# Kernel tuning notes

Hardware: AMD Instinct MI355X
Metric: run time of the kernel (lower is better)

## Reference

```python
import jax, jax.numpy as jnp
import numpy as np

B, N, HID, H, DH, NB = 4, 4096, 768, 12, 64, 266
EPS = 1e-4


def softmax_kernel(data, proj, is_query):
    # data: [B,H,N,DH], proj: [NB,DH]. FAVOR+ positive softmax features.
    d = data.shape[-1]
    ratio = proj.shape[0] ** -0.5
    dn = d ** -0.25  # data normalizer
    data_dash = jnp.einsum('bhnd,jd->bhnj', data * dn, proj)  # [B,H,N,NB]
    diag = 0.5 * jnp.sum((data * dn) ** 2, axis=-1, keepdims=True)  # [B,H,N,1]
    if is_query:
        m = jnp.max(data_dash, axis=-1, keepdims=True)
    else:
        m = jnp.max(data_dash, axis=(-1, -2), keepdims=True)
    return ratio * (jnp.exp(data_dash - diag - m) + EPS)


def setup_inputs() -> dict:
    key = jax.random.key(0)
    ks = jax.random.split(key, 8)
    s = HID ** -0.5
    return {
        'hidden_states': jax.random.normal(ks[0], (B, N, HID), jnp.float32),
        'Wq': jax.random.normal(ks[1], (HID, HID), jnp.float32) * s,
        'bq': jnp.zeros((HID,), jnp.float32),
        'Wk': jax.random.normal(ks[2], (HID, HID), jnp.float32) * s,
        'bk': jnp.zeros((HID,), jnp.float32),
        'Wv': jax.random.normal(ks[3], (HID, HID), jnp.float32) * s,
        'bv': jnp.zeros((HID,), jnp.float32),
        'proj': jax.random.normal(ks[4], (NB, DH), jnp.float32),
    }


def reference(hidden_states, Wq, bq, Wk, bk, Wv, bv, proj):
    def heads(x):  # [B,N,HID] -> [B,H,N,DH]
        return x.reshape(B, N, H, DH).transpose(0, 2, 1, 3)

    q = heads(hidden_states @ Wq.T + bq)
    k = heads(hidden_states @ Wk.T + bk)
    v = heads(hidden_states @ Wv.T + bv)

    qp = softmax_kernel(q, proj, True)   # [B,H,N,NB]
    kp = softmax_kernel(k, proj, False)  # [B,H,N,NB]

    # non-causal linear attention: out = q' (k'^T v) / (q' sum_n k')
    k_sum = jnp.sum(kp, axis=2)                               # [B,H,NB]
    d_inv = 1.0 / jnp.einsum('bhnj,bhj->bhn', qp, k_sum)      # [B,H,N]
    ctx = jnp.einsum('bhnj,bhnd->bhjd', kp, v)                # [B,H,NB,DH]
    out = jnp.einsum('bhnj,bhjd->bhnd', qp, ctx) * d_inv[..., None]

    return out.transpose(0, 2, 1, 3).reshape(B, N, HID)
```

## Files before the change

kernel.cpp:

```cpp
#include <hip/hip_runtime.h>
#include <hip/hip_bf16.h>
#include <stdint.h>

#define B_   4
#define N_   4096
#define HID_ 768
#define H_   12
#define DH_  64
#define NB_  266
#define NBP_ 288
#define EPS_ 1e-4f
#define RATIO_ 0.06131393f
#define CSL_  ((size_t)48 * DH_ * NBP_)
#define KSL_  ((size_t)48 * NBP_)

typedef unsigned short u16;
typedef __attribute__((ext_vector_type(8))) short short8;
typedef __attribute__((ext_vector_type(4))) float floatx4;

__device__ __forceinline__ u16 f2b(float f) {
  __hip_bfloat16 h = __float2bfloat16(f);
  return *reinterpret_cast<u16*>(&h);
}
__device__ __forceinline__ float b2f(u16 u) {
  union { unsigned u; float f; } x; x.u = ((unsigned)u) << 16; return x.f;
}
__device__ __forceinline__ unsigned fmap(float x) {
  unsigned u = __float_as_uint(x);
  return (u & 0x80000000u) ? ~u : (u | 0x80000000u);
}
__device__ __forceinline__ float funmap(unsigned u) {
  unsigned b = (u & 0x80000000u) ? (u & 0x7FFFFFFFu) : ~u;
  return __uint_as_float(b);
}
__device__ __forceinline__ void gl16(const u16* g, u16* l) {
  __builtin_amdgcn_global_load_lds(
      (const __attribute__((address_space(1))) void*)g,
      (__attribute__((address_space(3))) void*)l, 16, 0, 0);
}

__global__ __launch_bounds__(256) void k_prep(
    const float4* __restrict__ hs, const float4* __restrict__ Wq,
    const float4* __restrict__ Wk, const float4* __restrict__ Wv,
    const float* __restrict__ proj,
    uint2* __restrict__ hsb, uint2* __restrict__ wb3, u16* __restrict__ projb,
    float* __restrict__ Vdz, unsigned* __restrict__ mbuf) {
  int blk = blockIdx.x;
  const int t = threadIdx.x;
  if (blk < 12288) {
    int i = blk * 256 + t;
    float4 v = hs[i];
    union { u16 s[4]; uint2 u; } pk;
    pk.s[0] = f2b(v.x); pk.s[1] = f2b(v.y); pk.s[2] = f2b(v.z); pk.s[3] = f2b(v.w);
    hsb[i] = pk.u;
    return;
  }
  blk -= 12288;
  if (blk < 1728) {
    int i = blk * 256 + t;
    int sel = i / 147456, j = i - sel * 147456;
    const float4* s = (sel == 0) ? Wq : (sel == 1) ? Wk : Wv;
    float4 v = s[j];
    union { u16 s4[4]; uint2 u; } pk;
    pk.s4[0] = f2b(v.x); pk.s4[1] = f2b(v.y); pk.s4[2] = f2b(v.z); pk.s4[3] = f2b(v.w);
    wb3[i] = pk.u;
    return;
  }
  blk -= 1728;
  if (blk < 72) {
    int i = blk * 256 + t;
    int j = i / DH_, d = i - j * DH_;
    float v = (j < NB_) ? proj[j * DH_ + d] * 0.35355339059327373f : 0.f;
    projb[i] = f2b(v);
    return;
  }
  blk -= 72;
  if (blk < 12) {
    int i = blk * 256 + t;
    Vdz[i] = 0.f;
    return;
  }
  if (t < B_ * H_) mbuf[t] = 0u;
}

__global__ __launch_bounds__(256) void k_qkv3(
    const u16* __restrict__ hsb, const u16* __restrict__ wb,
    const float* __restrict__ bq, const float* __restrict__ bk, const float* __restrict__ bv,
    u16* __restrict__ qb, u16* __restrict__ kb, u16* __restrict__ vT,
    float* __restrict__ diagk, float* __restrict__ Vd) {
  __shared__ u16 lds[3 * 8192];
  const int m0 = blockIdx.x * 128;
  const int bn = blockIdx.y;
  const int sel = bn / 6;
  const int or0 = (bn % 6) * 128;
  const u16* W = wb + (size_t)sel * HID_ * HID_;
  const int t = threadIdx.x, lane = t & 63, wv = t >> 6;
  const int lm = lane & 15, lq = lane >> 4;
  const int wr = (wv >> 1) * 64, wc = (wv & 1) * 64;
  const int srow = t >> 2;
  const int scol = ((t & 3) ^ ((t >> 3) & 3)) * 8;
  const u16* gA0 = hsb + (size_t)(m0 + srow) * HID_ + scol;
  const u16* gB0 = W + (size_t)(or0 + srow) * HID_ + scol;
  u16* lb = lds + wv * 512;
  const int slotc = (lq ^ ((lm >> 1) & 3)) * 8;
  const int aoff = (wr + lm) * 32 + slotc;
  const int boff = 4096 + (wc + lm) * 32 + slotc;

  floatx4 acc[4][4];
#pragma unroll
  for (int mt = 0; mt < 4; mt++)
#pragma unroll
    for (int nt = 0; nt < 4; nt++) acc[mt][nt] = (floatx4){0.f, 0.f, 0.f, 0.f};

#define STAGE_QKV(kt)                                            \
  {                                                              \
    const int k0_ = (kt) * 32;                                   \
    u16* l_ = lb + ((kt) % 3) * 8192;                            \
    gl16(gA0 + k0_, l_);                                         \
    gl16(gA0 + 64 * HID_ + k0_, l_ + 2048);                      \
    gl16(gB0 + k0_, l_ + 4096);                                  \
    gl16(gB0 + 64 * HID_ + k0_, l_ + 6144);                      \
  }

  STAGE_QKV(0);
  STAGE_QKV(1);
  asm volatile("s_waitcnt vmcnt(4)" ::: "memory");
  __builtin_amdgcn_s_barrier();

  for (int kt = 0; kt < 24; ++kt) {
    if (kt + 2 < 24) STAGE_QKV(kt + 2);
    const u16* bufA = lds + (kt % 3) * 8192;
    short8 af[4], bf[4];
#pragma unroll
    for (int mt = 0; mt < 4; mt++) af[mt] = *(const short8*)&bufA[aoff + mt * 512];
#pragma unroll
    for (int nt = 0; nt < 4; nt++) bf[nt] = *(const short8*)&bufA[boff + nt * 512];
    __builtin_amdgcn_s_setprio(1);
#pragma unroll
    for (int mt = 0; mt < 4; mt++)
#pragma unroll
      for (int nt = 0; nt < 4; nt++)
        acc[mt][nt] = __builtin_amdgcn_mfma_f32_16x16x32_bf16(af[mt], bf[nt], acc[mt][nt], 0, 0, 0);
    __builtin_amdgcn_s_setprio(0);
    if (kt < 22) asm volatile("s_waitcnt vmcnt(4)" ::: "memory");
    else         asm volatile("s_waitcnt vmcnt(0)" ::: "memory");
    __builtin_amdgcn_s_barrier();
  }
#undef STAGE_QKV

  if (sel == 0) {
#pragma unroll
    for (int nt = 0; nt < 4; nt++) {
      int lc = or0 + wc + nt * 16 + lm;
      float bb = bq[lc];
#pragma unroll
      for (int mt = 0; mt < 4; mt++) {
        int rowb = m0 + wr + mt * 16 + lq * 4;
#pragma unroll
        for (int r = 0; r < 4; r++)
          qb[(size_t)(rowb + r) * HID_ + lc] = f2b(acc[mt][nt][r] + bb);
      }
    }
  } else if (sel == 1) {
    float dsq[4][4];
#pragma unroll
    for (int mt = 0; mt < 4; mt++)
#pragma unroll
      for (int r = 0; r < 4; r++) dsq[mt][r] = 0.f;
#pragma unroll
    for (int nt = 0; nt < 4; nt++) {
      int lc = or0 + wc + nt * 16 + lm;
      float bb = bk[lc];
#pragma unroll
      for (int mt = 0; mt < 4; mt++) {
        int rowb = m0 + wr + mt * 16 + lq * 4;
#pragma unroll
        for (int r = 0; r < 4; r++) {
          u16 hv = f2b(acc[mt][nt][r] + bb);
          kb[(size_t)(rowb + r) * HID_ + lc] = hv;
          float fv = b2f(hv);
          dsq[mt][r] += fv * fv;
        }
      }
    }
    const int bh0 = (m0 >> 12) * H_ + ((or0 + wc) >> 6);
#pragma unroll
    for (int mt = 0; mt < 4; mt++)
#pragma unroll
      for (int r = 0; r < 4; r++) {
        float v = dsq[mt][r];
        v += __shfl_xor(v, 1); v += __shfl_xor(v, 2);
        v += __shfl_xor(v, 4); v += __shfl_xor(v, 8);
        if (lm == 0) {
          int rowb = m0 + wr + mt * 16 + lq * 4 + r;
          diagk[(size_t)bh0 * N_ + (rowb & 4095)] = 0.0625f * v;
        }
      }
  } else {
    const int hh = (or0 + wc) >> 6;
#pragma unroll
    for (int nt = 0; nt < 4; nt++) {
      int lc = or0 + wc + nt * 16 + lm;
      int dv = nt * 16 + lm;
      float bb = bv[lc];
      float vs = 0.f;
#pragma unroll
      for (int mt = 0; mt < 4; mt++) {
        int rowbase = m0 + wr + mt * 16 + lq * 4;
        int b = rowbase >> 12, n = rowbase & 4095;
        union { u16 s[4]; uint2 u; } pk;
#pragma unroll
        for (int r = 0; r < 4; r++) {
          float fv = acc[mt][nt][r] + bb;
          vs += fv;
          pk.s[r] = f2b(fv);
        }
        *(uint2*)(vT + ((size_t)(b * H_ + hh) * DH_ + dv) * N_ + n) = pk.u;
      }
      vs += __shfl_xor(vs, 16);
      vs += __shfl_xor(vs, 32);
      if (lq == 0) atomicAdd(&Vd[((m0 >> 12) * H_ + hh) * DH_ + dv], vs);
    }
  }
}

__global__ __launch_bounds__(256) void k_ctx6(
    const u16* __restrict__ kb, const u16* __restrict__ vT, const u16* __restrict__ projb,
    const float* __restrict__ diagk,
    float* __restrict__ ksumS8, float* __restrict__ ctxTf8, unsigned* __restrict__ mbuf) {
  __shared__ u16 kpl[32 * 72];
  __shared__ float kred[4][2][16];
  const int orig = blockIdx.x;
  const int lg = (orig & 7) * 432 + (orig >> 3);
  const int bhjb = lg >> 3, ns = lg & 7;
  const int bh = bhjb / 9, jb = bhjb - bh * 9;
  const int j0 = jb * 32;
  const int nbeg = ns * 512;
  const int b = bh / H_, h = bh - b * H_;
  const int t = threadIdx.x, lane = t & 63, wv = t >> 6;
  const int lm = lane & 15, lq = lane >> 4;
  const bool vj0 = (j0 + lm) < NB_;
  const bool vj1 = (j0 + 16 + lm) < NB_;
  short8 bp00, bp01, bp10, bp11;
  {
    const u16* pp = projb + (j0 + lm) * DH_ + lq * 8;
    bp00 = *(const short8*)pp;
    bp01 = *(const short8*)(pp + 32);
    pp += 16 * DH_;
    bp10 = *(const short8*)pp;
    bp11 = *(const short8*)(pp + 32);
  }
  const u16* kbB = kb + (size_t)(b * N_) * HID_ + h * DH_;
  const u16* vTb = vT + ((size_t)bh * DH_ + wv * 16 + lm) * N_;
  const float* dgB = diagk + (size_t)bh * N_;
  floatx4 acc0 = (floatx4){0.f,0.f,0.f,0.f}, acc1 = (floatx4){0.f,0.f,0.f,0.f};
  float kacc0 = 0.f, kacc1 = 0.f;
  float am = -3e38f;
  const u16* kr0 = kbB + (size_t)(nbeg + wv * 16 + lm) * HID_ + lq * 8;
  short8 af0 = *(const short8*)kr0;
  short8 af1 = *(const short8*)(kr0 + 32);
  floatx4 dg4 = *(const floatx4*)(dgB + nbeg + wv * 16 + lq * 4);

  for (int n64 = nbeg; n64 < nbeg + 512; n64 += 64) {
    __syncthreads();
    const int nn = (n64 + 64 < nbeg + 512) ? n64 + 64 : nbeg;
    const u16* krn = kbB + (size_t)(nn + wv * 16 + lm) * HID_ + lq * 8;
    short8 nf0 = *(const short8*)krn;
    short8 nf1 = *(const short8*)(krn + 32);
    floatx4 nd = *(const floatx4*)(dgB + nn + wv * 16 + lq * 4);
    short8 av0 = *(const short8*)(vTb + n64 + lq * 8);
    short8 av1 = *(const short8*)(vTb + n64 + 32 + lq * 8);
    {
      floatx4 a = __builtin_amdgcn_mfma_f32_16x16x32_bf16(af0, bp00, (floatx4){0.f,0.f,0.f,0.f}, 0, 0, 0);
      a = __builtin_amdgcn_mfma_f32_16x16x32_bf16(af1, bp01, a, 0, 0, 0);
      union { u16 s[4]; uint2 u; } pk;
      float kss = 0.f;
#pragma unroll
      for (int r = 0; r < 4; r++) {
        float tv = __expf(a[r] - dg4[r]);
        if (vj0) am = fmaxf(am, a[r]);
        kss += tv;
        pk.s[r] = f2b(tv);
      }
      kacc0 += kss;
      *(uint2*)&kpl[lm * 72 + wv * 16 + lq * 4] = pk.u;
      a = __builtin_amdgcn_mfma_f32_16x16x32_bf16(af0, bp10, (floatx4){0.f,0.f,0.f,0.f}, 0, 0, 0);
      a = __builtin_amdgcn_mfma_f32_16x16x32_bf16(af1, bp11, a, 0, 0, 0);
      kss = 0.f;
#pragma unroll
      for (int r = 0; r < 4; r++) {
        float tv = __expf(a[r] - dg4[r]);
        if (vj1) am = fmaxf(am, a[r]);
        kss += tv;
        pk.s[r] = f2b(tv);
      }
      kacc1 += kss;
      *(uint2*)&kpl[(16 + lm) * 72 + wv * 16 + lq * 4] = pk.u;
    }
    __syncthreads();
    {
      short8 bf = *(const short8*)&kpl[lm * 72 + lq * 8];
      acc0 = __builtin_amdgcn_mfma_f32_16x16x32_bf16(av0, bf, acc0, 0, 0, 0);
      bf = *(const short8*)&kpl[(16 + lm) * 72 + lq * 8];
      acc1 = __builtin_amdgcn_mfma_f32_16x16x32_bf16(av0, bf, acc1, 0, 0, 0);
      bf = *(const short8*)&kpl[lm * 72 + 32 + lq * 8];
      acc0 = __builtin_amdgcn_mfma_f32_16x16x32_bf16(av1, bf, acc0, 0, 0, 0);
      bf = *(const short8*)&kpl[(16 + lm) * 72 + 32 + lq * 8];
      acc1 = __builtin_amdgcn_mfma_f32_16x16x32_bf16(av1, bf, acc1, 0, 0, 0);
    }
    af0 = nf0; af1 = nf1; dg4 = nd;
  }
  {
    float v0 = kacc0; v0 += __shfl_xor(v0, 16); v0 += __shfl_xor(v0, 32);
    float v1 = kacc1; v1 += __shfl_xor(v1, 16); v1 += __shfl_xor(v1, 32);
    if (lq == 0) { kred[wv][0][lm] = v0; kred[wv][1][lm] = v1; }
  }
  __syncthreads();
  if (t < 32) {
    int jh = t >> 4, l = t & 15;
    ksumS8[(size_t)ns * KSL_ + bh * NBP_ + j0 + t] =
        kred[0][jh][l] + kred[1][jh][l] + kred[2][jh][l] + kred[3][jh][l];
  }
  {
    float* cb = ctxTf8 + (size_t)ns * CSL_ + ((size_t)bh * DH_ + wv * 16 + lq * 4) * NBP_ + j0 + lm;
#pragma unroll
    for (int r = 0; r < 4; r++) {
      cb[(size_t)r * NBP_] = acc0[r];
      cb[(size_t)r * NBP_ + 16] = acc1[r];
    }
  }
#pragma unroll
  for (int o = 1; o < 64; o <<= 1) am = fmaxf(am, __shfl_xor(am, o));
  if (lane == 0) atomicMax(&mbuf[bh], fmap(am));
}

__global__ __launch_bounds__(256) void k_fink(
    const float* __restrict__ ksumS8, const unsigned* __restrict__ mbuf,
    float* __restrict__ ksumf, float* __restrict__ Ck) {
  __shared__ float cks[4];
  const int bh = blockIdx.x;
  const int t = threadIdx.x;
  const float em = __expf(-funmap(mbuf[bh]));
  float ck = 0.f;
  for (int j = t; j < NBP_; j += 256) {
    const float* p = ksumS8 + bh * NBP_ + j;
    float s = p[0];
#pragma unroll
    for (int ns = 1; ns < 8; ns++) s += p[(size_t)ns * KSL_];
    float kv = (j < NB_) ? RATIO_ * (em * s + EPS_ * 4096.0f) : 0.f;
    ksumf[bh * NBP_ + j] = kv;
    ck += kv;
  }
#pragma unroll
  for (int o = 1; o < 64; o <<= 1) ck += __shfl_xor(ck, o);
  if ((t & 63) == 0) cks[t >> 6] = ck;
  __syncthreads();
  if (t == 0) Ck[bh] = ((cks[0] + cks[1]) + cks[2]) + cks[3];
}

__global__ __launch_bounds__(256) void k_finc(
    const float* __restrict__ ctxTf8, const float* __restrict__ Vd,
    const unsigned* __restrict__ mbuf,
    u16* __restrict__ ctxb, float* __restrict__ Cc) {
  __shared__ float red[4];
  const int d = blockIdx.x, bh = blockIdx.y;
  const int t = threadIdx.x;
  const float em = __expf(-funmap(mbuf[bh]));
  const float vd = Vd[bh * DH_ + d];
  const size_t rb = ((size_t)bh * DH_ + d) * NBP_;
  float csum = 0.f;
  for (int j = t; j < NBP_; j += 256) {
    const float* p = ctxTf8 + rb + j;
    float s = p[0];
#pragma unroll
    for (int ns = 1; ns < 8; ns++) s += p[(size_t)ns * CSL_];
    float c = (j < NB_) ? RATIO_ * (em * s + EPS_ * vd) : 0.f;
    csum += c;
    ctxb[rb + j] = f2b(c);
  }
#pragma unroll
  for (int o = 1; o < 64; o <<= 1) csum += __shfl_xor(csum, o);
  if ((t & 63) == 0) red[t >> 6] = csum;
  __syncthreads();
  if (t == 0) Cc[bh * DH_ + d] = ((red[0] + red[1]) + red[2]) + red[3];
}

__global__ __launch_bounds__(256) void k_out5(
    const u16* __restrict__ qb, const u16* __restrict__ projb,
    const u16* __restrict__ ctxb, const float* __restrict__ ksumf,
    const float* __restrict__ Cc, const float* __restrict__ Ck,
    float* __restrict__ outp) {
  __shared__ u16 qpl[4][16][296];
  const int bh = blockIdx.y, b = bh / H_, h = bh - b * H_;
  const int t = threadIdx.x, lane = t & 63, wv = t >> 6;
  const int lm = lane & 15, lq = lane >> 4;
  const int row0 = blockIdx.x * 64 + wv * 16;
  const u16* cb = ctxb + (size_t)bh * DH_ * NBP_;
  const float* ksb = ksumf + bh * NBP_;
  float ksv[17];
#pragma unroll
  for (int ct = 0; ct < 17; ct++) ksv[ct] = ksb[ct * 16 + lm];
  const float ckv = Ck[bh];

  const u16* prow = qb + (size_t)(b * N_ + row0 + lm) * HID_ + h * DH_ + lq * 8;
  short8 af0 = *(const short8*)prow;
  short8 af1 = *(const short8*)(prow + 32);
  float rs = 0.f;
#pragma unroll
  for (int i = 0; i < 8; i++) { float f = b2f(((const u16*)&af0)[i]); rs += f * f; }
#pragma unroll
  for (int i = 0; i < 8; i++) { float f = b2f(((const u16*)&af1)[i]); rs += f * f; }
  rs += __shfl_xor(rs, 16);
  rs += __shfl_xor(rs, 32);
  float dg[4];
#pragma unroll
  for (int r = 0; r < 4; r++) dg[r] = 0.0625f * __shfl(rs, lq * 4 + r);

  float tmax[4] = {0.f, 0.f, 0.f, 0.f};
  float skp[4] = {0.f, 0.f, 0.f, 0.f};
#pragma unroll
  for (int ct = 0; ct < 17; ct++) {
    const u16* pp = projb + (ct * 16 + lm) * DH_ + lq * 8;
    short8 bf0 = *(const short8*)pp;
    short8 bf1 = *(const short8*)(pp + 32);
    floatx4 a = __builtin_amdgcn_mfma_f32_16x16x32_bf16(af0, bf0, (floatx4){0.f,0.f,0.f,0.f}, 0, 0, 0);
    a = __builtin_amdgcn_mfma_f32_16x16x32_bf16(af1, bf1, a, 0, 0, 0);
    bool valid = (ct < 16) || (lm < 10);
#pragma unroll
    for (int r = 0; r < 4; r++) {
      float tv = __expf(a[r] - dg[r]);
      if (valid) tmax[r] = fmaxf(tmax[r], tv);
      skp[r] += tv * ksv[ct];
      qpl[wv][lq * 4 + r][ct * 16 + lm] = f2b(tv);
    }
  }
#pragma unroll
  for (int r = 0; r < 4; r++) qpl[wv][lq * 4 + r][272 + lm] = 0;
#pragma unroll
  for (int o = 1; o < 16; o <<= 1) {
#pragma unroll
    for (int r = 0; r < 4; r++) {
      tmax[r] = fmaxf(tmax[r], __shfl_xor(tmax[r], o));
      skp[r] += __shfl_xor(skp[r], o);
    }
  }
  float alpha[4], beta[4];
#pragma unroll
  for (int r = 0; r < 4; r++) {
    float s = __expf(-dg[r]) / tmax[r];
    float dinv = 1.f / (s * skp[r] + EPS_ * ckv);
    alpha[r] = s * dinv;
    beta[r] = EPS_ * dinv;
  }

  floatx4 ao[4];
#pragma unroll
  for (int dt = 0; dt < 4; dt++) ao[dt] = (floatx4){0.f, 0.f, 0.f, 0.f};
#pragma unroll
  for (int ks9 = 0; ks9 < 9; ks9++) {
    short8 aq = *(const short8*)&qpl[wv][lm][ks9 * 32 + lq * 8];
#pragma unroll
    for (int dt = 0; dt < 4; dt++) {
      short8 bc = *(const short8*)(cb + (size_t)(dt * 16 + lm) * NBP_ + ks9 * 32 + lq * 8);
      ao[dt] = __builtin_amdgcn_mfma_f32_16x16x32_bf16(aq, bc, ao[dt], 0, 0, 0);
    }
  }
#pragma unroll
  for (int dt = 0; dt < 4; dt++) {
    float ccd = Cc[bh * DH_ + dt * 16 + lm];
#pragma unroll
    for (int r = 0; r < 4; r++) {
      int n = row0 + lq * 4 + r;
      outp[((size_t)(b * N_ + n)) * HID_ + h * DH_ + dt * 16 + lm] =
          ao[dt][r] * alpha[r] + ccd * beta[r];
    }
  }
}

extern "C" void kernel_launch(void* const* d_in, const int* in_sizes, int n_in,
                              void* d_out, int out_size, void* d_ws, size_t ws_size,
                              hipStream_t stream) {
  (void)in_sizes; (void)n_in; (void)out_size; (void)ws_size;
  const float* hs   = (const float*)d_in[0];
  const float* Wq   = (const float*)d_in[1];
  const float* bq   = (const float*)d_in[2];
  const float* Wk   = (const float*)d_in[3];
  const float* bk   = (const float*)d_in[4];
  const float* Wv   = (const float*)d_in[5];
  const float* bv   = (const float*)d_in[6];
  const float* proj = (const float*)d_in[7];

  char* w = (char*)d_ws;
  u16* hsb   = (u16*)w;  w += (size_t)16384 * 768 * 2;
  u16* wb3   = (u16*)w;  w += (size_t)3 * 768 * 768 * 2;
  u16* projb = (u16*)w;  w += (size_t)NBP_ * 64 * 2;
  u16* qb    = (u16*)w;  w += (size_t)16384 * 768 * 2;
  u16* kb    = (u16*)w;  w += (size_t)16384 * 768 * 2;
  u16* vT    = (u16*)w;  w += (size_t)48 * DH_ * N_ * 2;
  float* ksumS8 = (float*)w; w += (size_t)8 * KSL_ * 4;
  float* ksumf  = (float*)w; w += (size_t)48 * NBP_ * 4;
  float* diagk  = (float*)w; w += (size_t)48 * N_ * 4;
  float* ctxTf8 = (float*)w; w += (size_t)8 * CSL_ * 4;
  u16* ctxTb = (u16*)w;  w += (size_t)48 * DH_ * NBP_ * 2;
  float* Vd   = (float*)w; w += (size_t)48 * DH_ * 4;
  float* Cc   = (float*)w; w += (size_t)48 * DH_ * 4;
  float* Ck   = (float*)w; w += (size_t)48 * 4;
  unsigned* mbuf = (unsigned*)w;

  hipLaunchKernelGGL(k_prep, dim3(14101), dim3(256), 0, stream,
                     (const float4*)hs, (const float4*)Wq, (const float4*)Wk, (const float4*)Wv,
                     proj, (uint2*)hsb, (uint2*)wb3, projb, Vd, mbuf);
  hipLaunchKernelGGL(k_qkv3, dim3(128, 18), dim3(256), 0, stream, hsb, wb3, bq, bk, bv, qb, kb, vT, diagk, Vd);
  hipLaunchKernelGGL(k_ctx6, dim3(3456), dim3(256), 0, stream, kb, vT, projb, diagk, ksumS8, ctxTf8, mbuf);
  hipLaunchKernelGGL(k_fink, dim3(48), dim3(256), 0, stream, ksumS8, mbuf, ksumf, Ck);
  hipLaunchKernelGGL(k_finc, dim3(64, 48), dim3(256), 0, stream, ctxTf8, Vd, mbuf, ctxTb, Cc);
  hipLaunchKernelGGL(k_out5, dim3(64, 48), dim3(256), 0, stream, qb, projb, ctxTb, ksumf, Cc, Ck, (float*)d_out);
}
```

Before: 377.6 us.

## Split output kernel work across waves by feature and head-dim tiles

The output kernel now gives each block 16 rows instead of 64. The four waves share those rows: each wave computes a strided subset of the 17 random-feature tiles into one shared qp tile, and the row max and normaliser are combined through shared memory after a barrier. Each wave then produces one 16-wide head-dim slice of the output, so the grid grows fourfold and per-thread register use drops. In exchange it adds a block barrier and shared-memory reductions, and the q rows and their diagonal term are reloaded redundantly by every wave.

```diff
diff --git a/kernel.cpp b/kernel.cpp
--- a/kernel.cpp
+++ b/kernel.cpp
@@ -385,21 +385,20 @@
   if (t == 0) Cc[bh * DH_ + d] = ((red[0] + red[1]) + red[2]) + red[3];
 }
 
-__global__ __launch_bounds__(256) void k_out5(
+__global__ __launch_bounds__(256) void k_out6(
     const u16* __restrict__ qb, const u16* __restrict__ projb,
     const u16* __restrict__ ctxb, const float* __restrict__ ksumf,
     const float* __restrict__ Cc, const float* __restrict__ Ck,
     float* __restrict__ outp) {
-  __shared__ u16 qpl[4][16][296];
+  __shared__ u16 qpl[16][296];
+  __shared__ float sred[4][16];
+  __shared__ float tred[4][16];
   const int bh = blockIdx.y, b = bh / H_, h = bh - b * H_;
   const int t = threadIdx.x, lane = t & 63, wv = t >> 6;
   const int lm = lane & 15, lq = lane >> 4;
-  const int row0 = blockIdx.x * 64 + wv * 16;
+  const int row0 = blockIdx.x * 16;
   const u16* cb = ctxb + (size_t)bh * DH_ * NBP_;
   const float* ksb = ksumf + bh * NBP_;
-  float ksv[17];
-#pragma unroll
-  for (int ct = 0; ct < 17; ct++) ksv[ct] = ksb[ct * 16 + lm];
   const float ckv = Ck[bh];
 
   const u16* prow = qb + (size_t)(b * N_ + row0 + lm) * HID_ + h * DH_ + lq * 8;
@@ -418,24 +417,26 @@
 
   float tmax[4] = {0.f, 0.f, 0.f, 0.f};
   float skp[4] = {0.f, 0.f, 0.f, 0.f};
-#pragma unroll
-  for (int ct = 0; ct < 17; ct++) {
+  for (int ct = wv; ct < 17; ct += 4) {
     const u16* pp = projb + (ct * 16 + lm) * DH_ + lq * 8;
     short8 bf0 = *(const short8*)pp;
     short8 bf1 = *(const short8*)(pp + 32);
     floatx4 a = __builtin_amdgcn_mfma_f32_16x16x32_bf16(af0, bf0, (floatx4){0.f,0.f,0.f,0.f}, 0, 0, 0);
     a = __builtin_amdgcn_mfma_f32_16x16x32_bf16(af1, bf1, a, 0, 0, 0);
     bool valid = (ct < 16) || (lm < 10);
+    float kv = ksb[ct * 16 + lm];
 #pragma unroll
     for (int r = 0; r < 4; r++) {
       float tv = __expf(a[r] - dg[r]);
       if (valid) tmax[r] = fmaxf(tmax[r], tv);
-      skp[r] += tv * ksv[ct];
-      qpl[wv][lq * 4 + r][ct * 16 + lm] = f2b(tv);
-    }
-  }
-#pragma unroll
-  for (int r = 0; r < 4; r++) qpl[wv][lq * 4 + r][272 + lm] = 0;
+      skp[r] += tv * kv;
+      qpl[lq * 4 + r][ct * 16 + lm] = f2b(tv);
+    }
+  }
+  if (wv == 0) {
+#pragma unroll
+    for (int r = 0; r < 4; r++) qpl[lq * 4 + r][272 + lm] = 0;
+  }
 #pragma unroll
   for (int o = 1; o < 16; o <<= 1) {
 #pragma unroll
@@ -444,36 +445,36 @@
       skp[r] += __shfl_xor(skp[r], o);
     }
   }
+  if (lm == 0) {
+#pragma unroll
+    for (int r = 0; r < 4; r++) { sred[wv][lq * 4 + r] = skp[r]; tred[wv][lq * 4 + r] = tmax[r]; }
+  }
+  __syncthreads();
   float alpha[4], beta[4];
 #pragma unroll
   for (int r = 0; r < 4; r++) {
-    float s = __expf(-dg[r]) / tmax[r];
-    float dinv = 1.f / (s * skp[r] + EPS_ * ckv);
+    int row = lq * 4 + r;
+    float sk = ((sred[0][row] + sred[1][row]) + sred[2][row]) + sred[3][row];
+    float tm = fmaxf(fmaxf(tred[0][row], tred[1][row]), fmaxf(tred[2][row], tred[3][row]));
+    float s = __expf(-dg[r]) / tm;
+    float dinv = 1.f / (s * sk + EPS_ * ckv);
     alpha[r] = s * dinv;
     beta[r] = EPS_ * dinv;
   }
 
-  floatx4 ao[4];
-#pragma unroll
-  for (int dt = 0; dt < 4; dt++) ao[dt] = (floatx4){0.f, 0.f, 0.f, 0.f};
+  floatx4 ao = (floatx4){0.f, 0.f, 0.f, 0.f};
 #pragma unroll
   for (int ks9 = 0; ks9 < 9; ks9++) {
-    short8 aq = *(const short8*)&qpl[wv][lm][ks9 * 32 + lq * 8];
-#pragma unroll
-    for (int dt = 0; dt < 4; dt++) {
-      short8 bc = *(const short8*)(cb + (size_t)(dt * 16 + lm) * NBP_ + ks9 * 32 + lq * 8);
-      ao[dt] = __builtin_amdgcn_mfma_f32_16x16x32_bf16(aq, bc, ao[dt], 0, 0, 0);
-    }
-  }
-#pragma unroll
-  for (int dt = 0; dt < 4; dt++) {
-    float ccd = Cc[bh * DH_ + dt * 16 + lm];
-#pragma unroll
-    for (int r = 0; r < 4; r++) {
-      int n = row0 + lq * 4 + r;
-      outp[((size_t)(b * N_ + n)) * HID_ + h * DH_ + dt * 16 + lm] =
-          ao[dt][r] * alpha[r] + ccd * beta[r];
-    }
+    short8 aq = *(const short8*)&qpl[lm][ks9 * 32 + lq * 8];
+    short8 bc = *(const short8*)(cb + (size_t)(wv * 16 + lm) * NBP_ + ks9 * 32 + lq * 8);
+    ao = __builtin_amdgcn_mfma_f32_16x16x32_bf16(aq, bc, ao, 0, 0, 0);
+  }
+  float ccd = Cc[bh * DH_ + wv * 16 + lm];
+#pragma unroll
+  for (int r = 0; r < 4; r++) {
+    int n = row0 + lq * 4 + r;
+    outp[((size_t)(b * N_ + n)) * HID_ + h * DH_ + wv * 16 + lm] =
+        ao[r] * alpha[r] + ccd * beta[r];
   }
 }
 
@@ -514,5 +515,5 @@
   hipLaunchKernelGGL(k_ctx6, dim3(3456), dim3(256), 0, stream, kb, vT, projb, diagk, ksumS8, ctxTf8, mbuf);
   hipLaunchKernelGGL(k_fink, dim3(48), dim3(256), 0, stream, ksumS8, mbuf, ksumf, Ck);
   hipLaunchKernelGGL(k_finc, dim3(64, 48), dim3(256), 0, stream, ctxTf8, Vd, mbuf, ctxTb, Cc);
-  hipLaunchKernelGGL(k_out5, dim3(64, 48), dim3(256), 0, stream, qb, projb, ctxTb, ksumf, Cc, Ck, (float*)d_out);
-}
+  hipLaunchKernelGGL(k_out6, dim3(256, 48), dim3(256), 0, stream, qb, projb, ctxTb, ksumf, Cc, Ck, (float*)d_out);
+}
```

After: 378.6 us. About the same (+0.3%).
